# Kernel optimization log

Measured on AMD Instinct MI355X. Metric: run time of the kernel, lower is better.

Reference implementation:

```python
import jax, jax.numpy as jnp
import numpy as np
import math

D_MODEL = 512
N_HEADS = 8
D_K = D_MODEL // N_HEADS
D_FF = 2048
EPS = 1e-6


def _layer_norm(x, gamma, beta):
    # Matches the torch module: unbiased std (ddof=1), divide by (std + eps)
    mean = jnp.mean(x, axis=-1, keepdims=True)
    std = jnp.std(x, axis=-1, ddof=1, keepdims=True)
    return gamma * (x - mean) / (std + EPS) + beta


def setup_inputs() -> dict:
    key = jax.random.key(0)
    ks = jax.random.split(key, 16)
    B, S = 4, 2048
    s_attn = 1.0 / math.sqrt(D_MODEL)
    s_ff1 = 1.0 / math.sqrt(D_MODEL)
    s_ff2 = 1.0 / math.sqrt(D_FF)
    inp = {
        "x": jax.random.normal(ks[0], (B, S, D_MODEL), dtype=jnp.float32),
        "mask": jnp.ones((1, 1, S, S), dtype=jnp.int32),
        "wq": jax.random.normal(ks[1], (D_MODEL, D_MODEL), jnp.float32) * s_attn,
        "bq": jnp.zeros((D_MODEL,), jnp.float32),
        "wk": jax.random.normal(ks[2], (D_MODEL, D_MODEL), jnp.float32) * s_attn,
        "bk": jnp.zeros((D_MODEL,), jnp.float32),
        "wv": jax.random.normal(ks[3], (D_MODEL, D_MODEL), jnp.float32) * s_attn,
        "bv": jnp.zeros((D_MODEL,), jnp.float32),
        "wo": jax.random.normal(ks[4], (D_MODEL, D_MODEL), jnp.float32) * s_attn,
        "bo": jnp.zeros((D_MODEL,), jnp.float32),
        "w1": jax.random.normal(ks[5], (D_MODEL, D_FF), jnp.float32) * s_ff1,
        "b1": jnp.zeros((D_FF,), jnp.float32),
        "w2": jax.random.normal(ks[6], (D_FF, D_MODEL), jnp.float32) * s_ff2,
        "b2": jnp.zeros((D_MODEL,), jnp.float32),
        "g1": jnp.ones((1, 1, D_MODEL), jnp.float32),
        "be1": jnp.zeros((1, 1, D_MODEL), jnp.float32),
        "g2": jnp.ones((1, 1, D_MODEL), jnp.float32),
        "be2": jnp.zeros((1, 1, D_MODEL), jnp.float32),
    }
    return inp


def reference(x, mask, wq, bq, wk, bk, wv, bv, wo, bo, w1, b1, w2, b2, g1, be1, g2, be2):
    B, S, _ = x.shape
    # --- residual 1: pre-norm self-attention ---
    xn = _layer_norm(x, g1, be1)
    q = (xn @ wq + bq).reshape(B, S, N_HEADS, D_K).transpose(0, 2, 1, 3)
    k = (xn @ wk + bk).reshape(B, S, N_HEADS, D_K).transpose(0, 2, 1, 3)
    v = (xn @ wv + bv).reshape(B, S, N_HEADS, D_K).transpose(0, 2, 1, 3)
    # NOTE: source uses floor division `//` by sqrt(d_k) (a faithful-ly kept bug)
    scores = jnp.floor_divide(jnp.einsum("bhqd,bhkd->bhqk", q, k), math.sqrt(D_K))
    scores = jnp.where(mask == 0, jnp.float32(-1e9), scores)
    attn = jax.nn.softmax(scores, axis=-1)
    ctx = jnp.einsum("bhqk,bhkd->bhqd", attn, v)
    ctx = ctx.transpose(0, 2, 1, 3).reshape(B, S, D_MODEL)
    x = x + (ctx @ wo + bo)
    # --- residual 2: pre-norm feed-forward ---
    xn2 = _layer_norm(x, g2, be2)
    ff = jax.nn.relu(xn2 @ w1 + b1) @ w2 + b2
    return x + ff
```

## Files before the change

### kernel.cpp

```cpp
#include <hip/hip_runtime.h>
#include <cmath>

#define SEQ 2048
#define DM 512
#define DFF 2048
#define NH 8
#define DKH 64
#define NROWS 8192

typedef __attribute__((ext_vector_type(8))) short bf16x8;
typedef __attribute__((ext_vector_type(16))) float f32x16;

__device__ __forceinline__ ushort f2bf(float f) {
    uint u = __float_as_uint(f);
    u += 0x7fff + ((u >> 16) & 1);
    return (ushort)(u >> 16);
}
__device__ __forceinline__ float bf2f(ushort h) {
    return __uint_as_float(((uint)h) << 16);
}
__device__ __forceinline__ uint cvtpk_bf16(float a, float b) {
    uint r;
    asm("v_cvt_pk_bf16_f32 %0, %1, %2" : "=v"(r) : "v"(a), "v"(b));
    return r;
}
__device__ __forceinline__ void gl_lds16(const void* g, void* l) {
    __builtin_amdgcn_global_load_lds(
        (const __attribute__((address_space(1))) void*)g,
        (__attribute__((address_space(3))) void*)l, 16, 0, 0);
}
__device__ __forceinline__ void* swz(char* base, int row, int col) {
    int byte = (row << 7) + (col << 1);
    byte ^= (row & 7) << 4;
    return base + byte;
}
__device__ __forceinline__ void* swzg(char* base, int row, int k) {
    int byte = (row << 7) + (k << 1);
    byte ^= ((row >> 2) & 7) << 4;
    return base + byte;
}

template<bool SPLIT>
__global__ __launch_bounds__(256) void ln_kernel(const float* __restrict__ x,
        const float* __restrict__ g, const float* __restrict__ b,
        ushort* __restrict__ oh, ushort* __restrict__ ol) {
    int row = blockIdx.x * 4 + (threadIdx.x >> 6);
    int t = threadIdx.x & 63;
    const float* xr = x + (size_t)row * DM + t * 8;
    float v[8];
    *(float4*)&v[0] = *(const float4*)(xr);
    *(float4*)&v[4] = *(const float4*)(xr + 4);
    float s = 0.f;
    #pragma unroll
    for (int j = 0; j < 8; ++j) s += v[j];
    #pragma unroll
    for (int m = 32; m > 0; m >>= 1) s += __shfl_xor(s, m);
    float mean = s * (1.0f / DM);
    float ss = 0.f;
    #pragma unroll
    for (int j = 0; j < 8; ++j) { float d = v[j] - mean; ss += d * d; }
    #pragma unroll
    for (int m = 32; m > 0; m >>= 1) ss += __shfl_xor(ss, m);
    float inv = 1.0f / (sqrtf(ss * (1.0f / (DM - 1))) + 1e-6f);
    float gv[8], bv[8];
    *(float4*)&gv[0] = *(const float4*)(g + t * 8);
    *(float4*)&gv[4] = *(const float4*)(g + t * 8 + 4);
    *(float4*)&bv[0] = *(const float4*)(b + t * 8);
    *(float4*)&bv[4] = *(const float4*)(b + t * 8 + 4);
    union { ushort us[8]; float4 f4; } ph, pl;
    #pragma unroll
    for (int j = 0; j < 8; ++j) {
        float o = gv[j] * (v[j] - mean) * inv + bv[j];
        ushort hb = f2bf(o);
        ph.us[j] = hb;
        if (SPLIT) pl.us[j] = f2bf(o - bf2f(hb));
    }
    *(float4*)(oh + (size_t)row * DM + t * 8) = ph.f4;
    if (SPLIT) *(float4*)(ol + (size_t)row * DM + t * 8) = pl.f4;
}

__global__ __launch_bounds__(256) void prep(
        const float* __restrict__ wq, const float* __restrict__ wk,
        const float* __restrict__ wv, const float* __restrict__ wo,
        const float* __restrict__ w1, const float* __restrict__ w2,
        const int* __restrict__ mask,
        ushort* __restrict__ qh, ushort* __restrict__ ql,
        ushort* __restrict__ kh, ushort* __restrict__ kl,
        ushort* __restrict__ vh, ushort* __restrict__ oh,
        ushort* __restrict__ w1t, ushort* __restrict__ w2t,
        ushort* __restrict__ mb, unsigned char* __restrict__ mflag) {
    __shared__ float tile[64][65];
    int id = blockIdx.x;
    int t = threadIdx.x;
    if (id < 768) {
        const float* W;
        ushort* Th;
        ushort* Tl = nullptr;
        int K, N, k0, n0;
        bool split = false;
        if (id < 256) {
            int z = id >> 6, r = id & 63;
            W = (z == 0) ? wq : (z == 1) ? wk : (z == 2) ? wv : wo;
            Th = (z == 0) ? qh : (z == 1) ? kh : (z == 2) ? vh : oh;
            Tl = (z == 0) ? ql : (z == 1) ? kl : nullptr;
            split = (z < 2);
            K = DM; N = DM;
            k0 = (r >> 3) * 64; n0 = (r & 7) * 64;
        } else if (id < 512) {
            int r = id - 256;
            W = w1; Th = w1t; K = DM; N = DFF;
            k0 = (r & 7) * 64; n0 = (r >> 3) * 64;
        } else {
            int r = id - 512;
            W = w2; Th = w2t; K = DFF; N = DM;
            k0 = (r & 31) * 64; n0 = (r >> 5) * 64;
        }
        {
            int kr = t >> 2, c0 = (t & 3) * 16;
            const float* src = W + (size_t)(k0 + kr) * N + n0 + c0;
            #pragma unroll
            for (int j = 0; j < 4; ++j)
                *(float4*)&tile[kr][c0 + j * 4] = *(const float4*)(src + j * 4);
        }
        __syncthreads();
        int n = t >> 2, kc = (t & 3) * 16;
        union { ushort us[16]; float4 f4[2]; } ph, pl;
        #pragma unroll
        for (int j = 0; j < 16; ++j) {
            float v = tile[kc + j][n];
            ushort hb = f2bf(v);
            ph.us[j] = hb;
            pl.us[j] = f2bf(v - bf2f(hb));
        }
        ushort* dh = Th + (size_t)(n0 + n) * K + k0 + kc;
        *(float4*)(dh) = ph.f4[0];
        *(float4*)(dh + 8) = ph.f4[1];
        if (split) {
            ushort* dl = Tl + (size_t)(n0 + n) * K + k0 + kc;
            *(float4*)(dl) = pl.f4[0];
            *(float4*)(dl + 8) = pl.f4[1];
        }
    } else {
        int row = (id - 768) * 4 + (t >> 6);
        int lane = t & 63;
        ushort neg = f2bf(-1e9f);
        unsigned long long bal[4];
        #pragma unroll
        for (int u = 0; u < 4; ++u) {
            int base = row * SEQ + u * 512 + lane * 8;
            int4 a = *(const int4*)(mask + base);
            int4 c = *(const int4*)(mask + base + 4);
            union { ushort us[8]; float4 f4; } o;
            o.us[0] = a.x ? (ushort)0 : neg;
            o.us[1] = a.y ? (ushort)0 : neg;
            o.us[2] = a.z ? (ushort)0 : neg;
            o.us[3] = a.w ? (ushort)0 : neg;
            o.us[4] = c.x ? (ushort)0 : neg;
            o.us[5] = c.y ? (ushort)0 : neg;
            o.us[6] = c.z ? (ushort)0 : neg;
            o.us[7] = c.w ? (ushort)0 : neg;
            *(float4*)(mb + base) = o.f4;
            bool ok = a.x && a.y && a.z && a.w && c.x && c.y && c.z && c.w;
            bal[u] = __ballot(ok);
        }
        if (lane < 32) {
            int u = lane >> 3;
            unsigned long long bsel = bal[0];
            bsel = (u == 1) ? bal[1] : bsel;
            bsel = (u == 2) ? bal[2] : bsel;
            bsel = (u == 3) ? bal[3] : bsel;
            int byte = (int)((bsel >> ((lane & 7) * 8)) & 0xFFull);
            mflag[row * 32 + lane] = (byte == 0xFF) ? 1 : 0;
        }
    }
}

__global__ __launch_bounds__(256) void vtrans(const ushort* __restrict__ vh,
        ushort* __restrict__ vt) {
    __shared__ __align__(16) char tile[8192];
    int s0 = blockIdx.x * 64;
    int bh = blockIdx.y;
    int b = bh >> 3, h = bh & 7;
    int t = threadIdx.x;
    {
        int r = t >> 2, co = (t & 3) * 16;
        const ushort* src = vh + (size_t)(b * SEQ + s0 + r) * DM + h * DKH + co;
        *(float4*)swz(tile, r, co) = *(const float4*)(src);
        *(float4*)swz(tile, r, co + 8) = *(const float4*)(src + 8);
    }
    __syncthreads();
    int d = t >> 2, j0 = (t & 3) * 16;
    union { ushort us[16]; float4 f4[2]; } o;
    #pragma unroll
    for (int j = 0; j < 16; ++j)
        o.us[j] = *(ushort*)swz(tile, j0 + j, d);
    ushort* dst = vt + ((size_t)bh * DKH + d) * SEQ + s0 + j0;
    *(float4*)(dst) = o.f4[0];
    *(float4*)(dst + 8) = o.f4[1];
}

template<bool RELU, bool HASRES, int OUT>
__global__ __launch_bounds__(256) void mgemm(
        const ushort* __restrict__ Ah, const ushort* __restrict__ Bth,
        const float* __restrict__ bias, const float* __restrict__ resid,
        float* __restrict__ Cf, ushort* __restrict__ Cbh,
        int M, int N, int K) {
    __shared__ __align__(16) char smem[65536];
    int tid = threadIdx.x;
    int lane = tid & 63, w = tid >> 6;
    int ln31 = lane & 31, hi = lane >> 5;
    int mh = (w >> 1) * 64, nh = (w & 1) * 64;
    int gx = gridDim.x;
    int nwg = gx * gridDim.y;
    int flat = blockIdx.y * gx + blockIdx.x;
    int sid = (flat & 7) * (nwg >> 3) + (flat >> 3);
    int n0 = (sid % gx) * 128;
    int m0 = (sid / gx) * 128;

    f32x16 acc[2][2];
    #pragma unroll
    for (int i = 0; i < 2; ++i)
        #pragma unroll
        for (int j = 0; j < 2; ++j)
            #pragma unroll
            for (int r = 0; r < 16; ++r) acc[i][j][r] = 0.f;

    auto stage = [&](char* Abuf, char* Bbuf, int k0) {
        #pragma unroll
        for (int c = 0; c < 4; ++c) {
            int ch = w * 4 + c;
            int r = ch * 8 + (lane >> 3);
            int u = (lane & 7) ^ ((r >> 2) & 7);
            gl_lds16(Ah + (size_t)(m0 + r) * K + k0 + u * 8, Abuf + ch * 1024);
            gl_lds16(Bth + (size_t)(n0 + r) * K + k0 + u * 8, Bbuf + ch * 1024);
        }
    };

    char* A0 = smem;
    char* B0 = smem + 16384;
    char* A1 = smem + 32768;
    char* B1 = smem + 49152;

    stage(A0, B0, 0);
    __syncthreads();
    int nk = K / 64;
    for (int kt = 0; kt < nk; ++kt) {
        char* Ac = (kt & 1) ? A1 : A0;
        char* Bc = (kt & 1) ? B1 : B0;
        if (kt + 1 < nk)
            stage((kt & 1) ? A0 : A1, (kt & 1) ? B0 : B1, (kt + 1) * 64);
        __builtin_amdgcn_s_setprio(1);
        #pragma unroll
        for (int km = 0; km < 4; ++km) {
            int kk = km * 16 + hi * 8;
            bf16x8 ah[2], bh[2];
            ah[0] = *(bf16x8*)swzg(Ac, mh + ln31, kk);
            ah[1] = *(bf16x8*)swzg(Ac, mh + 32 + ln31, kk);
            bh[0] = *(bf16x8*)swzg(Bc, nh + ln31, kk);
            bh[1] = *(bf16x8*)swzg(Bc, nh + 32 + ln31, kk);
            #pragma unroll
            for (int mi = 0; mi < 2; ++mi)
                #pragma unroll
                for (int ni = 0; ni < 2; ++ni)
                    acc[mi][ni] = __builtin_amdgcn_mfma_f32_32x32x16_bf16(
                        ah[mi], bh[ni], acc[mi][ni], 0, 0, 0);
        }
        __builtin_amdgcn_s_setprio(0);
        __syncthreads();
    }
    float bv[2];
    bv[0] = bias[n0 + nh + ln31];
    bv[1] = bias[n0 + nh + 32 + ln31];
    #pragma unroll
    for (int mi = 0; mi < 2; ++mi)
        #pragma unroll
        for (int ni = 0; ni < 2; ++ni) {
            int n = n0 + nh + ni * 32 + ln31;
            #pragma unroll
            for (int r = 0; r < 16; ++r) {
                int m = m0 + mh + mi * 32 + (r & 3) + 8 * (r >> 2) + 4 * hi;
                float v = acc[mi][ni][r] + bv[ni];
                if (HASRES) v += resid[(size_t)m * N + n];
                if (RELU) v = fmaxf(v, 0.f);
                size_t idx = (size_t)m * N + n;
                if (OUT == 0) Cf[idx] = v;
                else Cbh[idx] = f2bf(v);
            }
        }
}

template<bool RELU, bool HASRES, int OUT>
__global__ __launch_bounds__(256) void mgemm64(
        const ushort* __restrict__ Ah, const ushort* __restrict__ Bth,
        const float* __restrict__ bias, const float* __restrict__ resid,
        float* __restrict__ Cf, ushort* __restrict__ Cbh,
        int M, int N, int K) {
    __shared__ __align__(16) char smem[32768];
    int tid = threadIdx.x;
    int lane = tid & 63, w = tid >> 6;
    int ln31 = lane & 31, hi = lane >> 5;
    int mh = (w >> 1) * 32, nh = (w & 1) * 32;
    int gx = gridDim.x;
    int nwg = gx * gridDim.y;
    int flat = blockIdx.y * gx + blockIdx.x;
    int sid = (flat & 7) * (nwg >> 3) + (flat >> 3);
    int n0 = (sid % gx) * 64;
    int m0 = (sid / gx) * 64;

    f32x16 acc;
    #pragma unroll
    for (int r = 0; r < 16; ++r) acc[r] = 0.f;

    auto stage = [&](char* Abuf, char* Bbuf, int k0) {
        #pragma unroll
        for (int c = 0; c < 2; ++c) {
            int ch = w * 2 + c;
            int r = ch * 8 + (lane >> 3);
            int u = (lane & 7) ^ ((r >> 2) & 7);
            gl_lds16(Ah + (size_t)(m0 + r) * K + k0 + u * 8, Abuf + ch * 1024);
            gl_lds16(Bth + (size_t)(n0 + r) * K + k0 + u * 8, Bbuf + ch * 1024);
        }
    };

    char* A0 = smem;
    char* B0 = smem + 8192;
    char* A1 = smem + 16384;
    char* B1 = smem + 24576;

    stage(A0, B0, 0);
    __syncthreads();
    int nk = K / 64;
    for (int kt = 0; kt < nk; ++kt) {
        char* Ac = (kt & 1) ? A1 : A0;
        char* Bc = (kt & 1) ? B1 : B0;
        if (kt + 1 < nk)
            stage((kt & 1) ? A0 : A1, (kt & 1) ? B0 : B1, (kt + 1) * 64);
        __builtin_amdgcn_s_setprio(1);
        #pragma unroll
        for (int km = 0; km < 4; ++km) {
            int kk = km * 16 + hi * 8;
            bf16x8 a = *(bf16x8*)swzg(Ac, mh + ln31, kk);
            bf16x8 b = *(bf16x8*)swzg(Bc, nh + ln31, kk);
            acc = __builtin_amdgcn_mfma_f32_32x32x16_bf16(a, b, acc, 0, 0, 0);
        }
        __builtin_amdgcn_s_setprio(0);
        __syncthreads();
    }
    float bv = bias[n0 + nh + ln31];
    int n = n0 + nh + ln31;
    #pragma unroll
    for (int r = 0; r < 16; ++r) {
        int m = m0 + mh + (r & 3) + 8 * (r >> 2) + 4 * hi;
        float v = acc[r] + bv;
        if (HASRES) v += resid[(size_t)m * N + n];
        if (RELU) v = fmaxf(v, 0.f);
        size_t idx = (size_t)m * N + n;
        if (OUT == 0) Cf[idx] = v;
        else Cbh[idx] = f2bf(v);
    }
}

__global__ __launch_bounds__(256) void qkv_gemm(
        const ushort* __restrict__ Ah, const ushort* __restrict__ Al,
        const ushort* __restrict__ Bth, const ushort* __restrict__ Btl,
        const float* __restrict__ bq, const float* __restrict__ bk,
        const float* __restrict__ bv_, ushort* __restrict__ q_h,
        ushort* __restrict__ q_l, ushort* __restrict__ k_h,
        ushort* __restrict__ k_l, ushort* __restrict__ v_h) {
    const int K = DM, N = DM;
    __shared__ __align__(16) char smem[65536];
    char* As_h = smem;
    char* Bs_h = smem + 16384;
    char* As_l = smem + 32768;
    char* Bs_l = smem + 49152;
    int tid = threadIdx.x;
    int lane = tid & 63, w = tid >> 6;
    int ln31 = lane & 31, hi = lane >> 5;
    int mh = (w >> 1) * 64, nh = (w & 1) * 64;
    int gx = gridDim.x;
    int nwg = gx * gridDim.y;
    int flat = blockIdx.y * gx + blockIdx.x;
    int sid = (flat & 7) * (nwg >> 3) + (flat >> 3);
    int n0 = (sid % gx) * 128;
    int m0 = (sid / gx) * 128;
    bool isqk = (n0 < 1024);

    f32x16 acc[2][2];
    #pragma unroll
    for (int i = 0; i < 2; ++i)
        #pragma unroll
        for (int j = 0; j < 2; ++j)
            #pragma unroll
            for (int r = 0; r < 16; ++r) acc[i][j][r] = 0.f;

    for (int k0 = 0; k0 < K; k0 += 64) {
        #pragma unroll
        for (int c = 0; c < 4; ++c) {
            int ch = w * 4 + c;
            int r = ch * 8 + (lane >> 3);
            int u = (lane & 7) ^ ((r >> 2) & 7);
            gl_lds16(Ah + (size_t)(m0 + r) * K + k0 + u * 8, As_h + ch * 1024);
            gl_lds16(Bth + (size_t)(n0 + r) * K + k0 + u * 8, Bs_h + ch * 1024);
            if (isqk) {
                gl_lds16(Al + (size_t)(m0 + r) * K + k0 + u * 8, As_l + ch * 1024);
                gl_lds16(Btl + (size_t)(n0 + r) * K + k0 + u * 8, Bs_l + ch * 1024);
            }
        }
        __syncthreads();
        __builtin_amdgcn_s_setprio(1);
        #pragma unroll
        for (int km = 0; km < 4; ++km) {
            int kk = km * 16 + hi * 8;
            bf16x8 ah[2], bh[2];
            ah[0] = *(bf16x8*)swzg(As_h, mh + ln31, kk);
            ah[1] = *(bf16x8*)swzg(As_h, mh + 32 + ln31, kk);
            bh[0] = *(bf16x8*)swzg(Bs_h, nh + ln31, kk);
            bh[1] = *(bf16x8*)swzg(Bs_h, nh + 32 + ln31, kk);
            if (isqk) {
                bf16x8 al[2], bl[2];
                al[0] = *(bf16x8*)swzg(As_l, mh + ln31, kk);
                al[1] = *(bf16x8*)swzg(As_l, mh + 32 + ln31, kk);
                bl[0] = *(bf16x8*)swzg(Bs_l, nh + ln31, kk);
                bl[1] = *(bf16x8*)swzg(Bs_l, nh + 32 + ln31, kk);
                #pragma unroll
                for (int mi = 0; mi < 2; ++mi)
                    #pragma unroll
                    for (int ni = 0; ni < 2; ++ni) {
                        acc[mi][ni] = __builtin_amdgcn_mfma_f32_32x32x16_bf16(
                            ah[mi], bh[ni], acc[mi][ni], 0, 0, 0);
                        acc[mi][ni] = __builtin_amdgcn_mfma_f32_32x32x16_bf16(
                            ah[mi], bl[ni], acc[mi][ni], 0, 0, 0);
                        acc[mi][ni] = __builtin_amdgcn_mfma_f32_32x32x16_bf16(
                            al[mi], bh[ni], acc[mi][ni], 0, 0, 0);
                    }
            } else {
                #pragma unroll
                for (int mi = 0; mi < 2; ++mi)
                    #pragma unroll
                    for (int ni = 0; ni < 2; ++ni)
                        acc[mi][ni] = __builtin_amdgcn_mfma_f32_32x32x16_bf16(
                            ah[mi], bh[ni], acc[mi][ni], 0, 0, 0);
            }
        }
        __builtin_amdgcn_s_setprio(0);
        __syncthreads();
    }
    const float* bias = (n0 < 512) ? bq : (n0 < 1024 ? bk : bv_);
    int ncol0 = n0 & 511;
    ushort* Oh = (n0 < 512) ? q_h : (n0 < 1024 ? k_h : v_h);
    ushort* Ol = (n0 < 512) ? q_l : (n0 < 1024 ? k_l : nullptr);
    float scale = (n0 < 512) ? 0.125f : 1.0f;
    float bvv[2];
    bvv[0] = bias[ncol0 + nh + ln31];
    bvv[1] = bias[ncol0 + nh + 32 + ln31];
    #pragma unroll
    for (int mi = 0; mi < 2; ++mi)
        #pragma unroll
        for (int ni = 0; ni < 2; ++ni) {
            int n = ncol0 + nh + ni * 32 + ln31;
            #pragma unroll
            for (int r = 0; r < 16; ++r) {
                int m = m0 + mh + mi * 32 + (r & 3) + 8 * (r >> 2) + 4 * hi;
                float v = (acc[mi][ni][r] + bvv[ni]) * scale;
                size_t idx = (size_t)m * N + n;
                ushort hb = f2bf(v);
                Oh[idx] = hb;
                if (isqk) Ol[idx] = f2bf(v - bf2f(hb));
            }
        }
}

__global__ __launch_bounds__(512) void attn_kernel(
        const ushort* __restrict__ Qh, const ushort* __restrict__ Ql,
        const ushort* __restrict__ Khg, const ushort* __restrict__ Klg,
        const ushort* __restrict__ Vtg, const ushort* __restrict__ mb,
        const unsigned char* __restrict__ mflag,
        ushort* __restrict__ pctx0, ushort* __restrict__ pctx1,
        float2* __restrict__ ml) {
    __shared__ __align__(16) char smem[65536];
    int tid = threadIdx.x;
    int w = tid >> 6, lane = tid & 63;
    int ln31 = lane & 31, hi = lane >> 5;
    bool hib = (hi != 0);
    int f = blockIdx.y * gridDim.x + blockIdx.x;
    int g = (f & 7) * 64 + (f >> 3);
    int bh = g >> 4, rest = g & 15;
    int part = rest >> 3, qb = rest & 7;
    int b = bh >> 3, h = bh & 7;
    int q0 = qb * 256;
    size_t brow = (size_t)b * SEQ;
    int hcol = h * DKH;
    int ktbeg = part * 16, ktend = ktbeg + 16;

    auto stage_kv = [&](char* buf, int kt) {
        #pragma unroll
        for (int c = 0; c < 3; ++c) {
            int q = w * 3 + c;
            int reg = q >> 3;
            int r = (q & 7) * 8 + (lane >> 3);
            int u = (lane & 7) ^ (r & 7);
            const ushort* src;
            if (reg == 0)
                src = Khg + (brow + kt * 64 + r) * DM + hcol + u * 8;
            else if (reg == 1)
                src = Klg + (brow + kt * 64 + r) * DM + hcol + u * 8;
            else
                src = Vtg + ((size_t)bh * DKH + r) * SEQ + kt * 64 + u * 8;
            gl_lds16(src, buf + q * 1024);
        }
    };

    {
        char* QhL = smem;
        char* QlL = smem + 32768;
        #pragma unroll
        for (int c = 0; c < 4; ++c) {
            int ch = w * 4 + c;
            int r = ch * 8 + (lane >> 3);
            int u = (lane & 7) ^ (r & 7);
            gl_lds16(Qh + (brow + q0 + r) * DM + hcol + u * 8, QhL + ch * 1024);
            gl_lds16(Ql + (brow + q0 + r) * DM + hcol + u * 8, QlL + ch * 1024);
        }
    }
    __syncthreads();
    bf16x8 qfh[4], qfl[4];
    {
        int qr = w * 32 + ln31;
        #pragma unroll
        for (int c = 0; c < 4; ++c) {
            qfh[c] = *(bf16x8*)swz(smem, qr, c * 16 + hi * 8);
            qfl[c] = *(bf16x8*)swz(smem + 32768, qr, c * 16 + hi * 8);
        }
    }
    __syncthreads();
    stage_kv(smem + (ktbeg & 1) * 24576, ktbeg);
    __syncthreads();

    f32x16 ctx0, ctx1;
    #pragma unroll
    for (int r = 0; r < 16; ++r) { ctx0[r] = 0.f; ctx1[r] = 0.f; }
    float m_i = -1e30f, l_i = 0.f;
    int qglob = q0 + w * 32 + ln31;
    const ushort* mrow = mb + (size_t)qglob * SEQ;

    for (int kt = ktbeg; kt < ktend; ++kt) {
        char* cur = smem + (kt & 1) * 24576;
        if (kt + 1 < ktend)
            stage_kv(smem + ((kt + 1) & 1) * 24576, kt + 1);
        unsigned char fl = mflag[qglob * 32 + kt];
        bool domask = !__all(fl != 0);
        ushort4 mpre[8];
        if (domask) {
            #pragma unroll
            for (int i = 0; i < 8; ++i)
                mpre[i] = *(const ushort4*)(mrow + kt * 64 + i * 8 + hi * 4);
        }
        char* KhL = cur;
        char* KlL = cur + 8192;
        char* VtL = cur + 16384;
        #pragma unroll
        for (int ksub = 0; ksub < 2; ++ksub) {
            f32x16 s;
            #pragma unroll
            for (int r = 0; r < 16; ++r) s[r] = 0.f;
            __builtin_amdgcn_s_setprio(1);
            #pragma unroll
            for (int c = 0; c < 4; ++c) {
                bf16x8 ka = *(bf16x8*)swz(KhL, ksub * 32 + ln31, c * 16 + hi * 8);
                bf16x8 kb = *(bf16x8*)swz(KlL, ksub * 32 + ln31, c * 16 + hi * 8);
                s = __builtin_amdgcn_mfma_f32_32x32x16_bf16(ka, qfh[c], s, 0, 0, 0);
                s = __builtin_amdgcn_mfma_f32_32x32x16_bf16(ka, qfl[c], s, 0, 0, 0);
                s = __builtin_amdgcn_mfma_f32_32x32x16_bf16(kb, qfh[c], s, 0, 0, 0);
            }
            __builtin_amdgcn_s_setprio(0);
            float tmax = -1e30f;
            if (domask) {
                #pragma unroll
                for (int rg = 0; rg < 4; ++rg) {
                    ushort4 mv = mpre[ksub * 4 + rg];
                    ushort mu[4] = {mv.x, mv.y, mv.z, mv.w};
                    #pragma unroll
                    for (int j = 0; j < 4; ++j) {
                        int r = rg * 4 + j;
                        float sc = floorf(s[r]) + bf2f(mu[j]);
                        s[r] = sc;
                        tmax = fmaxf(tmax, sc);
                    }
                }
            } else {
                #pragma unroll
                for (int r = 0; r < 16; ++r) {
                    float sc = floorf(s[r]);
                    s[r] = sc;
                    tmax = fmaxf(tmax, sc);
                }
            }
            tmax = fmaxf(tmax, __shfl_xor(tmax, 32));
            if (!__all(tmax <= m_i)) {
                float newm = fmaxf(m_i, tmax);
                float scl = __expf(m_i - newm);
                m_i = newm;
                l_i *= scl;
                #pragma unroll
                for (int r = 0; r < 16; ++r) { ctx0[r] *= scl; ctx1[r] *= scl; }
            }
            float psum = 0.f;
            #pragma unroll
            for (int r = 0; r < 16; ++r) {
                float p = __expf(s[r] - m_i);
                s[r] = p;
                psum += p;
            }
            psum += __shfl_xor(psum, 32);
            l_i += psum;
            uint pk0[4], pk1[4];
            #pragma unroll
            for (int rg = 0; rg < 4; ++rg) {
                pk0[rg] = cvtpk_bf16(s[rg * 4 + 0], s[rg * 4 + 1]);
                pk1[rg] = cvtpk_bf16(s[rg * 4 + 2], s[rg * 4 + 3]);
            }
            bf16x8 pb[2];
            #pragma unroll
            for (int cc = 0; cc < 2; ++cc) {
                uint A0 = pk0[cc * 2], A1 = pk1[cc * 2];
                uint B0 = pk0[cc * 2 + 1], B1 = pk1[cc * 2 + 1];
                uint send0 = hib ? A0 : B0;
                uint send1 = hib ? A1 : B1;
                uint own0  = hib ? B0 : A0;
                uint own1  = hib ? B1 : A1;
                uint recv0 = (uint)__shfl_xor((int)send0, 32);
                uint recv1 = (uint)__shfl_xor((int)send1, 32);
                union { uint u[4]; bf16x8 v; } pbu;
                pbu.u[0] = hib ? recv0 : own0;
                pbu.u[1] = hib ? recv1 : own1;
                pbu.u[2] = hib ? own0 : recv0;
                pbu.u[3] = hib ? own1 : recv1;
                pb[cc] = pbu.v;
            }
            __builtin_amdgcn_s_setprio(1);
            #pragma unroll
            for (int cc = 0; cc < 2; ++cc) {
                int c = ksub * 2 + cc;
                bf16x8 va0 = *(bf16x8*)swz(VtL, ln31, c * 16 + hi * 8);
                bf16x8 va1 = *(bf16x8*)swz(VtL, 32 + ln31, c * 16 + hi * 8);
                ctx0 = __builtin_amdgcn_mfma_f32_32x32x16_bf16(va0, pb[cc], ctx0, 0, 0, 0);
                ctx1 = __builtin_amdgcn_mfma_f32_32x32x16_bf16(va1, pb[cc], ctx1, 0, 0, 0);
            }
            __builtin_amdgcn_s_setprio(0);
        }
        __syncthreads();
    }

    ushort* P = part ? pctx1 : pctx0;
    size_t pbase = ((size_t)bh * SEQ + qglob) * DKH;
    #pragma unroll
    for (int r = 0; r < 16; ++r) {
        int d = (r & 3) + 8 * (r >> 2) + 4 * hi;
        P[pbase + d] = f2bf(ctx0[r]);
        P[pbase + 32 + d] = f2bf(ctx1[r]);
    }
    if (hi == 0)
        ml[((size_t)part * 32 + bh) * SEQ + qglob] = make_float2(m_i, l_i);
}

__global__ __launch_bounds__(256) void attn_combine(
        const ushort* __restrict__ p0, const ushort* __restrict__ p1,
        const float2* __restrict__ ml, ushort* __restrict__ O) {
    int idx = blockIdx.x * 256 + threadIdx.x;
    int d0 = (idx & 7) * 8;
    int q = (idx >> 3) & (SEQ - 1);
    int bh = idx >> 14;
    int b = bh >> 3, h = bh & 7;
    size_t pb = ((size_t)bh * SEQ + q) * DKH + d0;
    bf16x8 c0 = *(const bf16x8*)(p0 + pb);
    bf16x8 c1 = *(const bf16x8*)(p1 + pb);
    float2 e0 = ml[(size_t)bh * SEQ + q];
    float2 e1 = ml[((size_t)32 + bh) * SEQ + q];
    float m = fmaxf(e0.x, e1.x);
    float w0 = __expf(e0.x - m), w1 = __expf(e1.x - m);
    float inv = 1.0f / (e0.y * w0 + e1.y * w1);
    union { ushort us[8]; float4 f4; } o;
    #pragma unroll
    for (int j = 0; j < 8; ++j) {
        float v0 = bf2f((ushort)c0[j]);
        float v1 = bf2f((ushort)c1[j]);
        o.us[j] = f2bf((v0 * w0 + v1 * w1) * inv);
    }
    *(float4*)(O + ((size_t)(b * SEQ + q)) * DM + h * DKH + d0) = o.f4;
}

extern "C" void kernel_launch(void* const* d_in, const int* in_sizes, int n_in,
                              void* d_out, int out_size, void* d_ws, size_t ws_size,
                              hipStream_t stream) {
    const float* x    = (const float*)d_in[0];
    const int*   mask = (const int*)d_in[1];
    const float* wq = (const float*)d_in[2];
    const float* bq = (const float*)d_in[3];
    const float* wk = (const float*)d_in[4];
    const float* bk = (const float*)d_in[5];
    const float* wv = (const float*)d_in[6];
    const float* bv = (const float*)d_in[7];
    const float* wo = (const float*)d_in[8];
    const float* bo = (const float*)d_in[9];
    const float* w1 = (const float*)d_in[10];
    const float* b1 = (const float*)d_in[11];
    const float* w2 = (const float*)d_in[12];
    const float* b2 = (const float*)d_in[13];
    const float* g1  = (const float*)d_in[14];
    const float* be1 = (const float*)d_in[15];
    const float* g2  = (const float*)d_in[16];
    const float* be2 = (const float*)d_in[17];
    float* out = (float*)d_out;

    char* ws = (char*)d_ws;
    const size_t MiB = 1024 * 1024;
    ushort* xn_h = (ushort*)(ws);
    ushort* xn_l = (ushort*)(ws + 8 * MiB);
    ushort* q_h  = (ushort*)(ws + 16 * MiB);
    ushort* q_l  = (ushort*)(ws + 24 * MiB);
    ushort* k_h  = (ushort*)(ws + 32 * MiB);
    ushort* k_l  = (ushort*)(ws + 40 * MiB);
    ushort* v_h  = (ushort*)(ws + 48 * MiB);
    ushort* v_t  = (ushort*)(ws + 56 * MiB);
    ushort* wqkvt_h = (ushort*)(ws + 64 * MiB);
    ushort* wqkvt_l = (ushort*)(ws + 66 * MiB);
    ushort* wot_h = (ushort*)(ws + 67 * MiB);
    unsigned char* mflag = (unsigned char*)(ws + 67 * MiB + 512 * 1024);
    ushort* w1t_h = (ushort*)(ws + 68 * MiB);
    ushort* w2t_h = (ushort*)(ws + 70 * MiB);
    ushort* mb    = (ushort*)(ws + 72 * MiB);
    ushort* pctx0 = (ushort*)(ws + 80 * MiB);
    ushort* pctx1 = (ushort*)(ws + 88 * MiB);
    float2* ml    = (float2*)(ws + 96 * MiB);
    ushort* ctx  = xn_h;
    ushort* xn2  = xn_l;
    ushort* ff1  = q_h;

    dim3 blk256(256);
    prep<<<1280, blk256, 0, stream>>>(
        wq, wk, wv, wo, w1, w2, mask,
        wqkvt_h, wqkvt_l, wqkvt_h + 512 * 512, wqkvt_l + 512 * 512,
        wqkvt_h + 1024 * 512, wot_h, w1t_h, w2t_h, mb, mflag);
    ln_kernel<true><<<NROWS / 4, blk256, 0, stream>>>(x, g1, be1, xn_h, xn_l);
    qkv_gemm<<<dim3(12, NROWS / 128), blk256, 0, stream>>>(
        xn_h, xn_l, wqkvt_h, wqkvt_l, bq, bk, bv, q_h, q_l, k_h, k_l, v_h);
    vtrans<<<dim3(SEQ / 64, 4 * NH), blk256, 0, stream>>>(v_h, v_t);
    {
        dim3 grid(32, 16);
        attn_kernel<<<grid, dim3(512), 0, stream>>>(
            q_h, q_l, k_h, k_l, v_t, mb, mflag, pctx0, pctx1, ml);
    }
    attn_combine<<<32 * SEQ * 8 / 256, blk256, 0, stream>>>(pctx0, pctx1, ml, ctx);
    {
        dim3 grid(DM / 64, NROWS / 64);
        mgemm64<false,true,0><<<grid, blk256, 0, stream>>>(
            ctx, wot_h, bo, x, out, nullptr, NROWS, DM, DM);
    }
    ln_kernel<false><<<NROWS / 4, blk256, 0, stream>>>(out, g2, be2, xn2, nullptr);
    {
        dim3 grid(DFF / 128, NROWS / 128);
        mgemm<true,false,1><<<grid, blk256, 0, stream>>>(
            xn2, w1t_h, b1, nullptr, nullptr, ff1, NROWS, DFF, DM);
    }
    {
        dim3 grid(DM / 64, NROWS / 64);
        mgemm64<false,true,0><<<grid, blk256, 0, stream>>>(
            ff1, w2t_h, b2, out, out, nullptr, NROWS, DM, DFF);
    }
}
```

Before: 233.8 us.

## Fuse LN1 into prep, V transpose into QKV epilogue, combine into out-proj

Merges the first layernorm into the prep kernel as extra blocks, writes V transposed directly from the QKV GEMM epilogue through a swizzled LDS staging tile, and folds the split-attention combine into the output-projection GEMM's A-tile load. This removes three kernel launches and the intermediate v_h and ctx round trips through global memory. The trade-off is that the out-proj GEMM now loads A synchronously through registers instead of with async global-to-LDS copies, and it recomputes the combine weights for every k-tile.

```diff
diff --git a/kernel.cpp b/kernel.cpp
--- a/kernel.cpp
+++ b/kernel.cpp
@@ -39,13 +39,16 @@
     byte ^= ((row >> 2) & 7) << 4;
     return base + byte;
 }
+__device__ __forceinline__ void* swzv(char* base, int row, int col) {
+    int byte = (row << 8) + (col << 1);
+    byte ^= (row & 7) << 4;
+    return base + byte;
+}
 
 template<bool SPLIT>
-__global__ __launch_bounds__(256) void ln_kernel(const float* __restrict__ x,
+__device__ __forceinline__ void ln_row(const float* __restrict__ x,
         const float* __restrict__ g, const float* __restrict__ b,
-        ushort* __restrict__ oh, ushort* __restrict__ ol) {
-    int row = blockIdx.x * 4 + (threadIdx.x >> 6);
-    int t = threadIdx.x & 63;
+        ushort* __restrict__ oh, ushort* __restrict__ ol, int row, int t) {
     const float* xr = x + (size_t)row * DM + t * 8;
     float v[8];
     *(float4*)&v[0] = *(const float4*)(xr);
@@ -79,16 +82,26 @@
     if (SPLIT) *(float4*)(ol + (size_t)row * DM + t * 8) = pl.f4;
 }
 
+template<bool SPLIT>
+__global__ __launch_bounds__(256) void ln_kernel(const float* __restrict__ x,
+        const float* __restrict__ g, const float* __restrict__ b,
+        ushort* __restrict__ oh, ushort* __restrict__ ol) {
+    ln_row<SPLIT>(x, g, b, oh, ol, blockIdx.x * 4 + (threadIdx.x >> 6),
+                  threadIdx.x & 63);
+}
+
 __global__ __launch_bounds__(256) void prep(
         const float* __restrict__ wq, const float* __restrict__ wk,
         const float* __restrict__ wv, const float* __restrict__ wo,
         const float* __restrict__ w1, const float* __restrict__ w2,
-        const int* __restrict__ mask,
+        const int* __restrict__ mask, const float* __restrict__ x,
+        const float* __restrict__ g1, const float* __restrict__ be1,
         ushort* __restrict__ qh, ushort* __restrict__ ql,
         ushort* __restrict__ kh, ushort* __restrict__ kl,
         ushort* __restrict__ vh, ushort* __restrict__ oh,
         ushort* __restrict__ w1t, ushort* __restrict__ w2t,
-        ushort* __restrict__ mb, unsigned char* __restrict__ mflag) {
+        ushort* __restrict__ mb, unsigned char* __restrict__ mflag,
+        ushort* __restrict__ xn_h, ushort* __restrict__ xn_l) {
     __shared__ float tile[64][65];
     int id = blockIdx.x;
     int t = threadIdx.x;
@@ -140,7 +153,7 @@
             *(float4*)(dl) = pl.f4[0];
             *(float4*)(dl + 8) = pl.f4[1];
         }
-    } else {
+    } else if (id < 1280) {
         int row = (id - 768) * 4 + (t >> 6);
         int lane = t & 63;
         ushort neg = f2bf(-1e9f);
@@ -172,31 +185,10 @@
             int byte = (int)((bsel >> ((lane & 7) * 8)) & 0xFFull);
             mflag[row * 32 + lane] = (byte == 0xFF) ? 1 : 0;
         }
-    }
-}
-
-__global__ __launch_bounds__(256) void vtrans(const ushort* __restrict__ vh,
-        ushort* __restrict__ vt) {
-    __shared__ __align__(16) char tile[8192];
-    int s0 = blockIdx.x * 64;
-    int bh = blockIdx.y;
-    int b = bh >> 3, h = bh & 7;
-    int t = threadIdx.x;
-    {
-        int r = t >> 2, co = (t & 3) * 16;
-        const ushort* src = vh + (size_t)(b * SEQ + s0 + r) * DM + h * DKH + co;
-        *(float4*)swz(tile, r, co) = *(const float4*)(src);
-        *(float4*)swz(tile, r, co + 8) = *(const float4*)(src + 8);
-    }
-    __syncthreads();
-    int d = t >> 2, j0 = (t & 3) * 16;
-    union { ushort us[16]; float4 f4[2]; } o;
-    #pragma unroll
-    for (int j = 0; j < 16; ++j)
-        o.us[j] = *(ushort*)swz(tile, j0 + j, d);
-    ushort* dst = vt + ((size_t)bh * DKH + d) * SEQ + s0 + j0;
-    *(float4*)(dst) = o.f4[0];
-    *(float4*)(dst + 8) = o.f4[1];
+    } else {
+        ln_row<true>(x, g1, be1, xn_h, xn_l,
+                     (id - 1280) * 4 + (t >> 6), t & 63);
+    }
 }
 
 template<bool RELU, bool HASRES, int OUT>
@@ -289,12 +281,13 @@
         }
 }
 
-template<bool RELU, bool HASRES, int OUT>
+template<bool RELU, bool HASRES, int OUT, bool COMB>
 __global__ __launch_bounds__(256) void mgemm64(
         const ushort* __restrict__ Ah, const ushort* __restrict__ Bth,
         const float* __restrict__ bias, const float* __restrict__ resid,
         float* __restrict__ Cf, ushort* __restrict__ Cbh,
-        int M, int N, int K) {
+        const ushort* __restrict__ p0, const ushort* __restrict__ p1,
+        const float2* __restrict__ mlp, int M, int N, int K) {
     __shared__ __align__(16) char smem[32768];
     int tid = threadIdx.x;
     int lane = tid & 63, w = tid >> 6;
@@ -317,7 +310,26 @@
             int ch = w * 2 + c;
             int r = ch * 8 + (lane >> 3);
             int u = (lane & 7) ^ ((r >> 2) & 7);
-            gl_lds16(Ah + (size_t)(m0 + r) * K + k0 + u * 8, Abuf + ch * 1024);
+            if (COMB) {
+                int m = m0 + r;
+                int b = m >> 11, q = m & (SEQ - 1);
+                int bh = b * 8 + (k0 >> 6);
+                size_t pbase = ((size_t)bh * SEQ + q) * DKH + u * 8;
+                union { ushort us[8]; float4 f4; } a0, a1, o;
+                a0.f4 = *(const float4*)(p0 + pbase);
+                a1.f4 = *(const float4*)(p1 + pbase);
+                float2 e0 = mlp[(size_t)bh * SEQ + q];
+                float2 e1 = mlp[((size_t)32 + bh) * SEQ + q];
+                float mm = fmaxf(e0.x, e1.x);
+                float w0 = __expf(e0.x - mm), w1 = __expf(e1.x - mm);
+                float inv = 1.0f / (e0.y * w0 + e1.y * w1);
+                #pragma unroll
+                for (int j = 0; j < 8; ++j)
+                    o.us[j] = f2bf((bf2f(a0.us[j]) * w0 + bf2f(a1.us[j]) * w1) * inv);
+                *(float4*)(Abuf + ch * 1024 + lane * 16) = o.f4;
+            } else {
+                gl_lds16(Ah + (size_t)(m0 + r) * K + k0 + u * 8, Abuf + ch * 1024);
+            }
             gl_lds16(Bth + (size_t)(n0 + r) * K + k0 + u * 8, Bbuf + ch * 1024);
         }
     };
@@ -366,7 +378,7 @@
         const float* __restrict__ bq, const float* __restrict__ bk,
         const float* __restrict__ bv_, ushort* __restrict__ q_h,
         ushort* __restrict__ q_l, ushort* __restrict__ k_h,
-        ushort* __restrict__ k_l, ushort* __restrict__ v_h) {
+        ushort* __restrict__ k_l, ushort* __restrict__ v_t) {
     const int K = DM, N = DM;
     __shared__ __align__(16) char smem[65536];
     char* As_h = smem;
@@ -445,29 +457,64 @@
         __builtin_amdgcn_s_setprio(0);
         __syncthreads();
     }
-    const float* bias = (n0 < 512) ? bq : (n0 < 1024 ? bk : bv_);
-    int ncol0 = n0 & 511;
-    ushort* Oh = (n0 < 512) ? q_h : (n0 < 1024 ? k_h : v_h);
-    ushort* Ol = (n0 < 512) ? q_l : (n0 < 1024 ? k_l : nullptr);
-    float scale = (n0 < 512) ? 0.125f : 1.0f;
-    float bvv[2];
-    bvv[0] = bias[ncol0 + nh + ln31];
-    bvv[1] = bias[ncol0 + nh + 32 + ln31];
-    #pragma unroll
-    for (int mi = 0; mi < 2; ++mi)
-        #pragma unroll
-        for (int ni = 0; ni < 2; ++ni) {
-            int n = ncol0 + nh + ni * 32 + ln31;
-            #pragma unroll
-            for (int r = 0; r < 16; ++r) {
-                int m = m0 + mh + mi * 32 + (r & 3) + 8 * (r >> 2) + 4 * hi;
-                float v = (acc[mi][ni][r] + bvv[ni]) * scale;
-                size_t idx = (size_t)m * N + n;
-                ushort hb = f2bf(v);
-                Oh[idx] = hb;
-                if (isqk) Ol[idx] = f2bf(v - bf2f(hb));
-            }
-        }
+    if (isqk) {
+        const float* bias = (n0 < 512) ? bq : bk;
+        int ncol0 = n0 & 511;
+        ushort* Oh = (n0 < 512) ? q_h : k_h;
+        ushort* Ol = (n0 < 512) ? q_l : k_l;
+        float scale = (n0 < 512) ? 0.125f : 1.0f;
+        float bvv[2];
+        bvv[0] = bias[ncol0 + nh + ln31];
+        bvv[1] = bias[ncol0 + nh + 32 + ln31];
+        #pragma unroll
+        for (int mi = 0; mi < 2; ++mi)
+            #pragma unroll
+            for (int ni = 0; ni < 2; ++ni) {
+                int n = ncol0 + nh + ni * 32 + ln31;
+                #pragma unroll
+                for (int r = 0; r < 16; ++r) {
+                    int m = m0 + mh + mi * 32 + (r & 3) + 8 * (r >> 2) + 4 * hi;
+                    float v = (acc[mi][ni][r] + bvv[ni]) * scale;
+                    size_t idx = (size_t)m * N + n;
+                    ushort hb = f2bf(v);
+                    Oh[idx] = hb;
+                    Ol[idx] = f2bf(v - bf2f(hb));
+                }
+            }
+    } else {
+        int ncol0 = n0 & 511;
+        float bvv[2];
+        bvv[0] = bv_[ncol0 + nh + ln31];
+        bvv[1] = bv_[ncol0 + nh + 32 + ln31];
+        __syncthreads();
+        #pragma unroll
+        for (int mi = 0; mi < 2; ++mi)
+            #pragma unroll
+            for (int ni = 0; ni < 2; ++ni) {
+                int nloc = nh + ni * 32 + ln31;
+                #pragma unroll
+                for (int r = 0; r < 16; ++r) {
+                    int mloc = mh + mi * 32 + (r & 3) + 8 * (r >> 2) + 4 * hi;
+                    *(ushort*)swzv(smem, mloc, nloc) =
+                        f2bf(acc[mi][ni][r] + bvv[ni]);
+                }
+            }
+        __syncthreads();
+        int nloc = tid >> 1, half = tid & 1;
+        int nglob = ncol0 + nloc;
+        int h = nglob >> 6, d = nglob & 63;
+        int b = m0 >> 11;
+        int s0 = (m0 & (SEQ - 1)) + half * 64;
+        ushort* dst = v_t + (((size_t)(b * 8 + h) * DKH + d) * SEQ) + s0;
+        #pragma unroll
+        for (int gblk = 0; gblk < 8; ++gblk) {
+            union { ushort us[8]; float4 f4; } ov;
+            #pragma unroll
+            for (int j = 0; j < 8; ++j)
+                ov.us[j] = *(ushort*)swzv(smem, half * 64 + gblk * 8 + j, nloc);
+            *(float4*)(dst + gblk * 8) = ov.f4;
+        }
+    }
 }
 
 __global__ __launch_bounds__(512) void attn_kernel(
@@ -661,32 +708,6 @@
     }
     if (hi == 0)
         ml[((size_t)part * 32 + bh) * SEQ + qglob] = make_float2(m_i, l_i);
-}
-
-__global__ __launch_bounds__(256) void attn_combine(
-        const ushort* __restrict__ p0, const ushort* __restrict__ p1,
-        const float2* __restrict__ ml, ushort* __restrict__ O) {
-    int idx = blockIdx.x * 256 + threadIdx.x;
-    int d0 = (idx & 7) * 8;
-    int q = (idx >> 3) & (SEQ - 1);
-    int bh = idx >> 14;
-    int b = bh >> 3, h = bh & 7;
-    size_t pb = ((size_t)bh * SEQ + q) * DKH + d0;
-    bf16x8 c0 = *(const bf16x8*)(p0 + pb);
-    bf16x8 c1 = *(const bf16x8*)(p1 + pb);
-    float2 e0 = ml[(size_t)bh * SEQ + q];
-    float2 e1 = ml[((size_t)32 + bh) * SEQ + q];
-    float m = fmaxf(e0.x, e1.x);
-    float w0 = __expf(e0.x - m), w1 = __expf(e1.x - m);
-    float inv = 1.0f / (e0.y * w0 + e1.y * w1);
-    union { ushort us[8]; float4 f4; } o;
-    #pragma unroll
-    for (int j = 0; j < 8; ++j) {
-        float v0 = bf2f((ushort)c0[j]);
-        float v1 = bf2f((ushort)c1[j]);
-        o.us[j] = f2bf((v0 * w0 + v1 * w1) * inv);
-    }
-    *(float4*)(O + ((size_t)(b * SEQ + q)) * DM + h * DKH + d0) = o.f4;
 }
 
 extern "C" void kernel_launch(void* const* d_in, const int* in_sizes, int n_in,
@@ -720,7 +741,6 @@
     ushort* q_l  = (ushort*)(ws + 24 * MiB);
     ushort* k_h  = (ushort*)(ws + 32 * MiB);
     ushort* k_l  = (ushort*)(ws + 40 * MiB);
-    ushort* v_h  = (ushort*)(ws + 48 * MiB);
     ushort* v_t  = (ushort*)(ws + 56 * MiB);
     ushort* wqkvt_h = (ushort*)(ws + 64 * MiB);
     ushort* wqkvt_l = (ushort*)(ws + 66 * MiB);
@@ -732,29 +752,26 @@
     ushort* pctx0 = (ushort*)(ws + 80 * MiB);
     ushort* pctx1 = (ushort*)(ws + 88 * MiB);
     float2* ml    = (float2*)(ws + 96 * MiB);
-    ushort* ctx  = xn_h;
     ushort* xn2  = xn_l;
     ushort* ff1  = q_h;
 
     dim3 blk256(256);
-    prep<<<1280, blk256, 0, stream>>>(
-        wq, wk, wv, wo, w1, w2, mask,
+    prep<<<3328, blk256, 0, stream>>>(
+        wq, wk, wv, wo, w1, w2, mask, x, g1, be1,
         wqkvt_h, wqkvt_l, wqkvt_h + 512 * 512, wqkvt_l + 512 * 512,
-        wqkvt_h + 1024 * 512, wot_h, w1t_h, w2t_h, mb, mflag);
-    ln_kernel<true><<<NROWS / 4, blk256, 0, stream>>>(x, g1, be1, xn_h, xn_l);
+        wqkvt_h + 1024 * 512, wot_h, w1t_h, w2t_h, mb, mflag, xn_h, xn_l);
     qkv_gemm<<<dim3(12, NROWS / 128), blk256, 0, stream>>>(
-        xn_h, xn_l, wqkvt_h, wqkvt_l, bq, bk, bv, q_h, q_l, k_h, k_l, v_h);
-    vtrans<<<dim3(SEQ / 64, 4 * NH), blk256, 0, stream>>>(v_h, v_t);
+        xn_h, xn_l, wqkvt_h, wqkvt_l, bq, bk, bv, q_h, q_l, k_h, k_l, v_t);
     {
         dim3 grid(32, 16);
         attn_kernel<<<grid, dim3(512), 0, stream>>>(
             q_h, q_l, k_h, k_l, v_t, mb, mflag, pctx0, pctx1, ml);
     }
-    attn_combine<<<32 * SEQ * 8 / 256, blk256, 0, stream>>>(pctx0, pctx1, ml, ctx);
     {
         dim3 grid(DM / 64, NROWS / 64);
-        mgemm64<false,true,0><<<grid, blk256, 0, stream>>>(
-            ctx, wot_h, bo, x, out, nullptr, NROWS, DM, DM);
+        mgemm64<false,true,0,true><<<grid, blk256, 0, stream>>>(
+            nullptr, wot_h, bo, x, out, nullptr, pctx0, pctx1, ml,
+            NROWS, DM, DM);
     }
     ln_kernel<false><<<NROWS / 4, blk256, 0, stream>>>(out, g2, be2, xn2, nullptr);
     {
@@ -764,7 +781,8 @@
     }
     {
         dim3 grid(DM / 64, NROWS / 64);
-        mgemm64<false,true,0><<<grid, blk256, 0, stream>>>(
-            ff1, w2t_h, b2, out, out, nullptr, NROWS, DM, DFF);
-    }
-}
+        mgemm64<false,true,0,false><<<grid, blk256, 0, stream>>>(
+            ff1, w2t_h, b2, out, out, nullptr, nullptr, nullptr, nullptr,
+            NROWS, DM, DFF);
+    }
+}
```

Measured after the change: 229.4 us. No clear change (-1.9%).
